# Optimization experiments

Hardware: AMD Instinct MI355X
Metric: run time of the kernel (lower is better)

Reference implementation:

```python
import jax, jax.numpy as jnp
import numpy as np
import math

D_MODEL = 1024
NUM_HEADS = 16
D_K = D_MODEL // NUM_HEADS
MAX_SEQ_LEN = 2048
THETA = 10000.0


def _make_rope_tables():
    inv_freq = 1.0 / (THETA ** (np.arange(0, D_K, 2, dtype=np.float32) / D_K))  # [D_K/2]
    pos = np.arange(MAX_SEQ_LEN, dtype=np.float32)
    freqs = np.einsum('i,j->ij', pos, inv_freq)                 # [S, D_K/2]
    dfreq = np.repeat(freqs, 2, axis=-1)                        # [S, D_K] (interleaved)
    return jnp.asarray(np.cos(dfreq)), jnp.asarray(np.sin(dfreq))


def setup_inputs() -> dict:
    key = jax.random.key(0)
    ks = jax.random.split(key, 5)
    std = math.sqrt(2.0 / (D_MODEL + D_MODEL))
    x = jax.random.normal(ks[0], (2, 2048, D_MODEL), dtype=jnp.float32)
    Wq = jax.random.truncated_normal(ks[1], -3.0, 3.0, (D_MODEL, D_MODEL), jnp.float32) * std
    Wk = jax.random.truncated_normal(ks[2], -3.0, 3.0, (D_MODEL, D_MODEL), jnp.float32) * std
    Wv = jax.random.truncated_normal(ks[3], -3.0, 3.0, (D_MODEL, D_MODEL), jnp.float32) * std
    Wo = jax.random.truncated_normal(ks[4], -3.0, 3.0, (D_MODEL, D_MODEL), jnp.float32) * std
    cos, sin = _make_rope_tables()
    token_positions = jnp.arange(2048, dtype=jnp.int32)
    return {"x": x, "Wq": Wq, "Wk": Wk, "Wv": Wv, "Wo": Wo,
            "cos": cos, "sin": sin, "token_positions": token_positions}


def _apply_rope(t, cos, sin, pos):
    # t: [B, H, S, D_K]; cos/sin gathered to [S, D_K], broadcast over B,H
    c = cos[pos]
    s = sin[pos]
    t1 = t[..., 0::2]
    t2 = t[..., 1::2]
    rot = jnp.stack((-t2, t1), axis=-1).reshape(t.shape)
    return t * c + rot * s


def reference(x, Wq, Wk, Wv, Wo, cos, sin, token_positions):
    B, S, _ = x.shape
    def heads(W):
        return (x @ W.T).reshape(B, S, NUM_HEADS, D_K).transpose(0, 2, 1, 3)  # [B,H,S,Dk]
    q = _apply_rope(heads(Wq), cos, sin, token_positions)
    k = _apply_rope(heads(Wk), cos, sin, token_positions)
    v = heads(Wv)
    scores = jnp.einsum('bhqd,bhkd->bhqk', q, k) / math.sqrt(D_K)
    causal = jnp.tril(jnp.ones((S, S), dtype=bool))
    scores = jnp.where(causal, scores, -jnp.inf)
    attn = jax.nn.softmax(scores, axis=-1)
    out = jnp.einsum('bhqk,bhkd->bhqd', attn, v)
    out = out.transpose(0, 2, 1, 3).reshape(B, S, D_MODEL)
    return out @ Wo.T
```

## Files before the change

### kernel.cpp

```cpp
#include <hip/hip_runtime.h>
#include <cstdint>
#include <cstddef>

#define D_MODEL 1024
#define NH 16
#define DK 64
#define S_LEN 2048

typedef __attribute__((ext_vector_type(8))) short bf16x8;
typedef __attribute__((ext_vector_type(4))) float f32x4;

#define QSCALE 0.1803368801111204f

__device__ __forceinline__ unsigned short f2bf(float f) {
    union { float f; unsigned int u; } v; v.f = f;
    unsigned int r = (v.u + 0x7fffu + ((v.u >> 16) & 1u)) >> 16;
    return (unsigned short)r;
}

#define GLL(g, l) __builtin_amdgcn_global_load_lds( \
    (const __attribute__((address_space(1))) unsigned int*)(g), \
    (__attribute__((address_space(3))) unsigned int*)(l), 16, 0, 0)

__global__ __launch_bounds__(256) void convert_bf16(
    const float* __restrict__ x,
    const float* __restrict__ wq, const float* __restrict__ wk,
    const float* __restrict__ wv, const float* __restrict__ wo,
    unsigned short* __restrict__ Xb, unsigned short* __restrict__ Wb,
    unsigned short* __restrict__ Wob)
{
    const unsigned t = blockIdx.x * 256 + threadIdx.x;
    const float* src;
    unsigned short* dst;
    if (t < 1048576u)      { src = x  + 4 * (size_t)t;               dst = Xb  + 4 * (size_t)t; }
    else if (t < 1310720u) { size_t i = t - 1048576u; src = wq + 4*i; dst = Wb + 4*i; }
    else if (t < 1572864u) { size_t i = t - 1310720u; src = wk + 4*i; dst = Wb + 1048576u + 4*i; }
    else if (t < 1835008u) { size_t i = t - 1572864u; src = wv + 4*i; dst = Wb + 2097152u + 4*i; }
    else                   { size_t i = t - 1835008u; src = wo + 4*i; dst = Wob + 4*i; }
    float4 v = *(const float4*)src;
    unsigned short pk[4] = {f2bf(v.x), f2bf(v.y), f2bf(v.z), f2bf(v.w)};
    *(uint2*)dst = *(const uint2*)pk;
}


#define CP 132
__global__ __launch_bounds__(256) void gemm_qkv(
    const unsigned short* __restrict__ Xb, const unsigned short* __restrict__ Wb,
    const float* __restrict__ cosT, const float* __restrict__ sinT,
    const int* __restrict__ posArr,
    unsigned short* __restrict__ Qo, unsigned short* __restrict__ Ko,
    unsigned short* __restrict__ Vt)
{
    __shared__ __align__(16) unsigned short smem[4 * 128 * 64];
    unsigned short* Cs = smem;

    const int tid  = threadIdx.x;
    const int wave = tid >> 6;
    const int lane = tid & 63;
    const int m16  = lane & 15;
    const int quad = lane >> 4;
    const int warpM = (wave >> 1) * 64;
    const int warpN = (wave & 1) * 64;
    const int rowBase = blockIdx.y * 128;
    const int colBase = blockIdx.x * 128;

    const int l8  = lane >> 3;
    const int lb  = lane & 7;
    const int cbl = (lb ^ l8) * 8;

    const unsigned short* Arow = Xb + (size_t)rowBase * D_MODEL;
    const unsigned short* Brow = Wb + (size_t)colBase * D_MODEL;

    f32x4 acc[4][4];
#pragma unroll
    for (int i = 0; i < 4; ++i)
#pragma unroll
        for (int j = 0; j < 4; ++j) acc[i][j] = (f32x4){0.f, 0.f, 0.f, 0.f};

    auto stage = [&](int k0, int bsel) {
        unsigned short* As = smem + bsel * 16384;
        unsigned short* Bs = As + 8192;
#pragma unroll
        for (int it = 0; it < 4; ++it) {
            const int r = wave * 32 + it * 8 + l8;
            const int dstOff = wave * 2048 + it * 512 + lane * 8;
            GLL(Arow + (size_t)r * D_MODEL + k0 + cbl, &As[dstOff]);
            GLL(Brow + (size_t)r * D_MODEL + k0 + cbl, &Bs[dstOff]);
        }
    };

    stage(0, 0);
    for (int it = 0; it < 16; ++it) {
        const int cur = it & 1;
        if (it < 15) {
            stage((it + 1) * 64, cur ^ 1);
            __asm__ volatile("s_waitcnt vmcnt(8)" ::: "memory");
        } else {
            __asm__ volatile("s_waitcnt vmcnt(0)" ::: "memory");
        }
        __syncthreads();
        const unsigned short* As = smem + cur * 16384;
        const unsigned short* Bs = As + 8192;
#pragma unroll
        for (int ks = 0; ks < 2; ++ks) {
            bf16x8 af[4], bf[4];
#pragma unroll
            for (int t4 = 0; t4 < 4; ++t4) {
                const int rowA = warpM + t4 * 16 + m16;
                const int rowB = warpN + t4 * 16 + m16;
                const int cb = ((ks * 4 + quad) ^ (m16 & 7)) * 8;
                af[t4] = *(const bf16x8*)&As[rowA * 64 + cb];
                bf[t4] = *(const bf16x8*)&Bs[rowB * 64 + cb];
            }
#pragma unroll
            for (int mt = 0; mt < 4; ++mt)
#pragma unroll
                for (int nt = 0; nt < 4; ++nt)
                    acc[mt][nt] = __builtin_amdgcn_mfma_f32_16x16x32_bf16(
                        af[mt], bf[nt], acc[mt][nt], 0, 0, 0);
        }
        __syncthreads();
    }

    const int which = (colBase + warpN) >> 10;
    if (which == 2) {
#pragma unroll
        for (int mt = 0; mt < 4; ++mt) {
            const int gr0 = rowBase + warpM + mt * 16 + quad * 4;
            const int b   = gr0 >> 11;
            const int s0  = gr0 & 2047;
#pragma unroll
            for (int nt = 0; nt < 4; ++nt) {
                const int c1 = (colBase + warpN + nt * 16 + m16) & 1023;
                const int h  = c1 >> 6;
                const int d  = c1 & 63;
                unsigned short pk[4];
#pragma unroll
                for (int r = 0; r < 4; ++r) pk[r] = f2bf(acc[mt][nt][r]);
                *(uint2*)(Vt + ((size_t)(b * NH + h) * DK + d) * S_LEN + s0) =
                    *(const uint2*)pk;
            }
        }
    } else {
#pragma unroll
        for (int mt = 0; mt < 4; ++mt) {
            const int lr0 = warpM + mt * 16 + quad * 4;
#pragma unroll
            for (int nt = 0; nt < 4; ++nt) {
                const int lc = warpN + nt * 16 + m16;
                const int d  = lc & 63;
#pragma unroll
                for (int r = 0; r < 4; ++r) {
                    const int s = (rowBase + lr0 + r) & 2047;
                    const int p = posArr[s];
                    float v = acc[mt][nt][r];
                    float o = __shfl_xor(v, 1, 64);
                    float c  = cosT[(size_t)p * DK + d];
                    float sn = sinT[(size_t)p * DK + d];
                    float res = (d & 1) ? (v * c + o * sn) : (v * c - o * sn);
                    if (which == 0) res *= QSCALE;
                    Cs[(lr0 + r) * CP + lc] = f2bf(res);
                }
            }
        }
        __syncthreads();
        unsigned short* outB = (which == 0) ? Qo : Ko;
        const int r2   = tid >> 1;
        const int half = tid & 1;
        const int gr   = rowBase + r2;
        const int b    = gr >> 11;
        const int s    = gr & 2047;
        const int h    = ((colBase & 1023) + half * 64) >> 6;
        unsigned short* dst = outB + ((size_t)(b * NH + h) * S_LEN + s) * DK;
        const unsigned short* srcp = &Cs[r2 * CP + half * 64];
#pragma unroll
        for (int j = 0; j < 8; ++j)
            ((uint4*)dst)[j] = ((const uint4*)srcp)[j];
    }
}

__global__ __launch_bounds__(256) void gemm_proj(
    const unsigned short* __restrict__ A, const unsigned short* __restrict__ B,
    float* __restrict__ C)
{
    __shared__ __align__(16) unsigned short smem[4 * 128 * 64];

    const int tid  = threadIdx.x;
    const int wave = tid >> 6;
    const int lane = tid & 63;
    const int m16  = lane & 15;
    const int quad = lane >> 4;
    const int warpM = (wave >> 1) * 64;
    const int warpN = (wave & 1) * 64;
    const int rowBase = blockIdx.y * 128;
    const int colBase = blockIdx.x * 128;

    const int l8  = lane >> 3;
    const int lb  = lane & 7;
    const int cbl = (lb ^ l8) * 8;

    const unsigned short* Arow = A + (size_t)rowBase * D_MODEL;
    const unsigned short* Brow = B + (size_t)colBase * D_MODEL;

    f32x4 acc[4][4];
#pragma unroll
    for (int i = 0; i < 4; ++i)
#pragma unroll
        for (int j = 0; j < 4; ++j) acc[i][j] = (f32x4){0.f, 0.f, 0.f, 0.f};

    auto stage = [&](int k0, int bsel) {
        unsigned short* As = smem + bsel * 16384;
        unsigned short* Bs = As + 8192;
#pragma unroll
        for (int it = 0; it < 4; ++it) {
            const int r = wave * 32 + it * 8 + l8;
            const int dstOff = wave * 2048 + it * 512 + lane * 8;
            GLL(Arow + (size_t)r * D_MODEL + k0 + cbl, &As[dstOff]);
            GLL(Brow + (size_t)r * D_MODEL + k0 + cbl, &Bs[dstOff]);
        }
    };

    stage(0, 0);
    for (int it = 0; it < 16; ++it) {
        const int cur = it & 1;
        if (it < 15) {
            stage((it + 1) * 64, cur ^ 1);
            __asm__ volatile("s_waitcnt vmcnt(8)" ::: "memory");
        } else {
            __asm__ volatile("s_waitcnt vmcnt(0)" ::: "memory");
        }
        __syncthreads();
        const unsigned short* As = smem + cur * 16384;
        const unsigned short* Bs = As + 8192;
#pragma unroll
        for (int ks = 0; ks < 2; ++ks) {
            bf16x8 af[4], bf[4];
#pragma unroll
            for (int t4 = 0; t4 < 4; ++t4) {
                const int rowA = warpM + t4 * 16 + m16;
                const int rowB = warpN + t4 * 16 + m16;
                const int cb = ((ks * 4 + quad) ^ (m16 & 7)) * 8;
                af[t4] = *(const bf16x8*)&As[rowA * 64 + cb];
                bf[t4] = *(const bf16x8*)&Bs[rowB * 64 + cb];
            }
#pragma unroll
            for (int mt = 0; mt < 4; ++mt)
#pragma unroll
                for (int nt = 0; nt < 4; ++nt)
                    acc[mt][nt] = __builtin_amdgcn_mfma_f32_16x16x32_bf16(
                        af[mt], bf[nt], acc[mt][nt], 0, 0, 0);
        }
        __syncthreads();
    }

#pragma unroll
    for (int mt = 0; mt < 4; ++mt)
#pragma unroll
        for (int reg = 0; reg < 4; ++reg) {
            int gr = rowBase + warpM + mt * 16 + quad * 4 + reg;
            float* crow = C + (size_t)gr * D_MODEL + colBase + warpN;
#pragma unroll
            for (int nt = 0; nt < 4; ++nt)
                crow[nt * 16 + m16] = acc[mt][nt][reg];
        }
}

__global__ __launch_bounds__(256, 3) void flash_mfma(
    const unsigned short* __restrict__ Q,
    const unsigned short* __restrict__ K,
    const unsigned short* __restrict__ Vt,
    unsigned short* __restrict__ O)
{
    const int g    = blockIdx.x;
    const int qt   = 31 - (g >> 5);
    const int bh   = g & 31;
    const int b    = bh >> 4;
    const int h    = bh & 15;
    const int tid  = threadIdx.x;
    const int wave = tid >> 6;
    const int lane = tid & 63;
    const int m16  = lane & 15;
    const int quad = lane >> 4;
    const int l8   = lane >> 3;
    const int nIter = (qt >> 1) + 1;

    __shared__ __align__(16) unsigned short Ks[128 * 64];
    __shared__ __align__(16) unsigned short VsT[64 * 128];
    __shared__ __align__(16) unsigned short Ps[64][136];

    const unsigned short* Qg = Q + ((size_t)bh * S_LEN + qt * 64) * DK;
#pragma unroll
    for (int it = 0; it < 2; ++it) {
        const int rb = wave * 16 + it * 8;
        const int r  = rb + l8;
        const int cb = ((lane & 7) ^ (r & 7)) * 8;
        GLL(Qg + r * DK + cb, &Ks[rb * 64 + lane * 8]);
    }
    __asm__ volatile("s_waitcnt vmcnt(0)" ::: "memory");
    __syncthreads();
    const int qrow = wave * 16 + m16;
    const bf16x8 qf0 = *(const bf16x8*)&Ks[qrow * 64 + ((quad ^ (m16 & 7)) * 8)];
    const bf16x8 qf1 = *(const bf16x8*)&Ks[qrow * 64 + (((4 + quad) ^ (m16 & 7)) * 8)];

    const short one_bf = (short)0x3F80;
    const bf16x8 ones8 = {one_bf, one_bf, one_bf, one_bf,
                          one_bf, one_bf, one_bf, one_bf};

    f32x4 o[4];
    f32x4 lacc = (f32x4){0.f, 0.f, 0.f, 0.f};
#pragma unroll
    for (int r = 0; r < 4; ++r) o[r] = (f32x4){0.f, 0.f, 0.f, 0.f};

    const unsigned short* Kg0 = K + (size_t)bh * S_LEN * DK;
    const unsigned short* Vg0 = Vt + (size_t)bh * DK * S_LEN;

    for (int kb = 0; kb < nIter; ++kb) {
        const int ko = kb * 128;
        __syncthreads();
#pragma unroll
        for (int it = 0; it < 4; ++it) {
            const int rb = wave * 32 + it * 8;
            const int r  = rb + l8;
            const int cb = ((lane & 7) ^ (r & 7)) * 8;
            GLL(Kg0 + (size_t)(ko + r) * DK + cb, &Ks[rb * 64 + lane * 8]);
        }
#pragma unroll
        for (int it = 0; it < 4; ++it) {
            const int db = wave * 16 + it * 4;
            const int d  = db + (lane >> 4);
            const int cb = ((lane & 15) ^ (d & 15)) * 8;
            GLL(Vg0 + (size_t)d * S_LEN + ko + cb, &VsT[db * 128 + lane * 8]);
        }
        __asm__ volatile("s_waitcnt vmcnt(0)" ::: "memory");
        __syncthreads();

        f32x4 s[8];
#pragma unroll
        for (int ct = 0; ct < 8; ++ct) {
            const int kr = ct * 16 + m16;
            bf16x8 kf0 = *(const bf16x8*)&Ks[kr * 64 + ((quad ^ (m16 & 7)) * 8)];
            bf16x8 kf1 = *(const bf16x8*)&Ks[kr * 64 + (((4 + quad) ^ (m16 & 7)) * 8)];
            f32x4 z = {0.f, 0.f, 0.f, 0.f};
            z = __builtin_amdgcn_mfma_f32_16x16x32_bf16(qf0, kf0, z, 0, 0, 0);
            z = __builtin_amdgcn_mfma_f32_16x16x32_bf16(qf1, kf1, z, 0, 0, 0);
            s[ct] = z;
        }

        if (kb == nIter - 1) {
#pragma unroll
            for (int ct = 0; ct < 8; ++ct)
#pragma unroll
                for (int r = 0; r < 4; ++r) {
                    int colk = ko + ct * 16 + m16;
                    int row  = qt * 64 + wave * 16 + quad * 4 + r;
                    if (colk > row) s[ct][r] = -16384.f;
                }
        }

#pragma unroll
        for (int ct = 0; ct < 8; ++ct)
#pragma unroll
            for (int r = 0; r < 4; ++r)
                Ps[wave * 16 + quad * 4 + r][ct * 16 + m16] =
                    f2bf(__builtin_exp2f(s[ct][r]));

        __asm__ volatile("s_waitcnt lgkmcnt(0)" ::: "memory");

        bf16x8 pf[4];
#pragma unroll
        for (int kc = 0; kc < 4; ++kc)
            pf[kc] = *(const bf16x8*)&Ps[wave * 16 + m16][kc * 32 + quad * 8];
#pragma unroll
        for (int kc = 0; kc < 4; ++kc)
            lacc = __builtin_amdgcn_mfma_f32_16x16x32_bf16(pf[kc], ones8, lacc, 0, 0, 0);
#pragma unroll
        for (int ct = 0; ct < 4; ++ct) {
            const int vr = ct * 16 + m16;
#pragma unroll
            for (int kc = 0; kc < 4; ++kc) {
                bf16x8 vf = *(const bf16x8*)
                    &VsT[vr * 128 + (((kc * 4 + quad) ^ m16) * 8)];
                o[ct] = __builtin_amdgcn_mfma_f32_16x16x32_bf16(pf[kc], vf, o[ct], 0, 0, 0);
            }
        }
    }

    float inv[4];
#pragma unroll
    for (int r = 0; r < 4; ++r) inv[r] = 1.0f / lacc[r];
#pragma unroll
    for (int r = 0; r < 4; ++r) {
        int srow = qt * 64 + wave * 16 + quad * 4 + r;
        unsigned short* orow = O + (((size_t)b * S_LEN + srow) * NH + h) * DK;
#pragma unroll
        for (int ct = 0; ct < 4; ++ct)
            orow[ct * 16 + m16] = f2bf(o[ct][r] * inv[r]);
    }
}

extern "C" void kernel_launch(void* const* d_in, const int* in_sizes, int n_in,
                              void* d_out, int out_size, void* d_ws, size_t ws_size,
                              hipStream_t stream)
{
    const float* x      = (const float*)d_in[0];
    const float* Wq     = (const float*)d_in[1];
    const float* Wk     = (const float*)d_in[2];
    const float* Wv     = (const float*)d_in[3];
    const float* Wo     = (const float*)d_in[4];
    const float* cosT   = (const float*)d_in[5];
    const float* sinT   = (const float*)d_in[6];
    const int*   posArr = (const int*)d_in[7];
    float* out = (float*)d_out;

    unsigned short* ws0 = (unsigned short*)d_ws;
    unsigned short* Xb  = ws0;
    unsigned short* Wb  = ws0 + 4194304;
    unsigned short* Wob = ws0 + 7340032;
    unsigned short* Qw  = ws0 + 8388608;
    unsigned short* Kw  = ws0 + 12582912;
    unsigned short* Vtw = ws0 + 16777216;
    unsigned short* Ow  = ws0 + 20971520;

    convert_bf16<<<8192, 256, 0, stream>>>(x, Wq, Wk, Wv, Wo, Xb, Wb, Wob);

    gemm_qkv<<<dim3(3072 / 128, 4096 / 128), 256, 0, stream>>>(
        Xb, Wb, cosT, sinT, posArr, Qw, Kw, Vtw);

    flash_mfma<<<1024, 256, 0, stream>>>(Qw, Kw, Vtw, Ow);

    gemm_proj<<<dim3(D_MODEL / 128, 4096 / 128), 256, 0, stream>>>(Ow, Wob, out);
}
```

Baseline: 201.5 us.

## Split long causal query tiles across two KV chunks and merge partials

The flash attention kernel now splits the eight longest query tiles per head into two KV-range chunks, launching 1280 blocks instead of 1024, with split tiles scheduled between the longest unsplit ones. Split blocks write unnormalized fp32 partial outputs and row sums to workspace, and a new merge kernel sums them and normalizes. This relies on the softmax using no running max, so partials add directly. It aims to shorten the tail from the heaviest causal blocks at the cost of an extra launch and fp32 partial traffic.

```diff
diff --git a/kernel.cpp b/kernel.cpp
--- a/kernel.cpp
+++ b/kernel.cpp
@@ -269,20 +269,38 @@
     const unsigned short* __restrict__ Q,
     const unsigned short* __restrict__ K,
     const unsigned short* __restrict__ Vt,
-    unsigned short* __restrict__ O)
+    unsigned short* __restrict__ O,
+    float* __restrict__ oP, float* __restrict__ lP)
 {
-    const int g    = blockIdx.x;
-    const int qt   = 31 - (g >> 5);
-    const int bh   = g & 31;
-    const int b    = bh >> 4;
-    const int h    = bh & 15;
+    const int g  = blockIdx.x;
+    const int j  = g >> 5;
+    const int bh = g & 31;
+    const int b  = bh >> 4;
+    const int h  = bh & 15;
+
+    int qt, kb0, kb1, chunk;
+    bool split;
+    if (j < 8) {
+        split = false; chunk = 0; qt = 23 - j;
+        kb0 = 0; kb1 = (qt >> 1) + 1;
+    } else if (j < 24) {
+        split = true; const int jj = j - 8;
+        qt = 24 + (jj >> 1); chunk = jj & 1;
+        const int nIt = (qt >> 1) + 1;
+        const int c0  = nIt >> 1;
+        kb0 = chunk ? c0 : 0; kb1 = chunk ? nIt : c0;
+    } else {
+        split = false; chunk = 0; qt = 39 - j;
+        kb0 = 0; kb1 = (qt >> 1) + 1;
+    }
+    const int nIterFull = (qt >> 1) + 1;
+
     const int tid  = threadIdx.x;
     const int wave = tid >> 6;
     const int lane = tid & 63;
     const int m16  = lane & 15;
     const int quad = lane >> 4;
     const int l8   = lane >> 3;
-    const int nIter = (qt >> 1) + 1;
 
     __shared__ __align__(16) unsigned short Ks[128 * 64];
     __shared__ __align__(16) unsigned short VsT[64 * 128];
@@ -314,7 +332,7 @@
     const unsigned short* Kg0 = K + (size_t)bh * S_LEN * DK;
     const unsigned short* Vg0 = Vt + (size_t)bh * DK * S_LEN;
 
-    for (int kb = 0; kb < nIter; ++kb) {
+    for (int kb = kb0; kb < kb1; ++kb) {
         const int ko = kb * 128;
         __syncthreads();
 #pragma unroll
@@ -346,7 +364,7 @@
             s[ct] = z;
         }
 
-        if (kb == nIter - 1) {
+        if (kb == nIterFull - 1) {
 #pragma unroll
             for (int ct = 0; ct < 8; ++ct)
 #pragma unroll
@@ -385,17 +403,64 @@
         }
     }
 
-    float inv[4];
-#pragma unroll
-    for (int r = 0; r < 4; ++r) inv[r] = 1.0f / lacc[r];
-#pragma unroll
-    for (int r = 0; r < 4; ++r) {
-        int srow = qt * 64 + wave * 16 + quad * 4 + r;
-        unsigned short* orow = O + (((size_t)b * S_LEN + srow) * NH + h) * DK;
-#pragma unroll
-        for (int ct = 0; ct < 4; ++ct)
-            orow[ct * 16 + m16] = f2bf(o[ct][r] * inv[r]);
-    }
+    if (!split) {
+        float inv[4];
+#pragma unroll
+        for (int r = 0; r < 4; ++r) inv[r] = 1.0f / lacc[r];
+#pragma unroll
+        for (int r = 0; r < 4; ++r) {
+            int srow = qt * 64 + wave * 16 + quad * 4 + r;
+            unsigned short* orow = O + (((size_t)b * S_LEN + srow) * NH + h) * DK;
+#pragma unroll
+            for (int ct = 0; ct < 4; ++ct)
+                orow[ct * 16 + m16] = f2bf(o[ct][r] * inv[r]);
+        }
+    } else {
+        const int slot = bh * 8 + (qt - 24);
+        float* ob = oP + ((size_t)chunk * 256 + slot) * 4096;
+        float* lb = lP + ((size_t)chunk * 256 + slot) * 64;
+#pragma unroll
+        for (int r = 0; r < 4; ++r) {
+            const int row = wave * 16 + quad * 4 + r;
+#pragma unroll
+            for (int ct = 0; ct < 4; ++ct)
+                ob[row * 64 + ct * 16 + m16] = o[ct][r];
+            if (m16 == 0) lb[row] = lacc[r];
+        }
+    }
+}
+
+__global__ __launch_bounds__(256) void flash_merge(
+    const float* __restrict__ oP, const float* __restrict__ lP,
+    unsigned short* __restrict__ O)
+{
+    const int slot = blockIdx.x;
+    const int bh   = slot >> 3;
+    const int qt   = (slot & 7) + 24;
+    const int b    = bh >> 4;
+    const int h    = bh & 15;
+    const int t    = threadIdx.x;
+    const int row  = t >> 2;
+    const int dp   = (t & 3) * 16;
+
+    const float* oA = oP + (size_t)slot * 4096 + row * 64 + dp;
+    const float* oB = oP + (size_t)(256 + slot) * 4096 + row * 64 + dp;
+    const float inv = 1.0f / (lP[slot * 64 + row] + lP[(256 + slot) * 64 + row]);
+
+    unsigned short pk[16];
+#pragma unroll
+    for (int i = 0; i < 16; i += 4) {
+        float4 a  = *(const float4*)(oA + i);
+        float4 bb = *(const float4*)(oB + i);
+        pk[i + 0] = f2bf((a.x + bb.x) * inv);
+        pk[i + 1] = f2bf((a.y + bb.y) * inv);
+        pk[i + 2] = f2bf((a.z + bb.z) * inv);
+        pk[i + 3] = f2bf((a.w + bb.w) * inv);
+    }
+    const int srow = qt * 64 + row;
+    unsigned short* dst = O + (((size_t)b * S_LEN + srow) * NH + h) * DK + dp;
+    ((uint4*)dst)[0] = ((const uint4*)pk)[0];
+    ((uint4*)dst)[1] = ((const uint4*)pk)[1];
 }
 
 extern "C" void kernel_launch(void* const* d_in, const int* in_sizes, int n_in,
@@ -420,13 +485,16 @@
     unsigned short* Kw  = ws0 + 12582912;
     unsigned short* Vtw = ws0 + 16777216;
     unsigned short* Ow  = ws0 + 20971520;
+    float* oP = (float*)(ws0 + 25165824);
+    float* lP = oP + 2 * 256 * 4096;
 
     convert_bf16<<<8192, 256, 0, stream>>>(x, Wq, Wk, Wv, Wo, Xb, Wb, Wob);
 
     gemm_qkv<<<dim3(3072 / 128, 4096 / 128), 256, 0, stream>>>(
         Xb, Wb, cosT, sinT, posArr, Qw, Kw, Vtw);
 
-    flash_mfma<<<1024, 256, 0, stream>>>(Qw, Kw, Vtw, Ow);
+    flash_mfma<<<1280, 256, 0, stream>>>(Qw, Kw, Vtw, Ow, oP, lP);
+    flash_merge<<<256, 256, 0, stream>>>(oP, lP, Ow);
 
     gemm_proj<<<dim3(D_MODEL / 128, 4096 / 128), 256, 0, stream>>>(Ow, Wob, out);
 }
```

Measured after the change: 204.3 us. No clear change (+1.4%).

## Keep softmax probabilities in registers by transposing the QK^T MFMA

Applied to the files above, without the earlier changes.

Swaps the MFMA operands for S = QK^T so each lane holds a column-major fragment of P that can feed the PV MFMA directly as the A operand. The P shared-memory buffer and its store/reload round trip are dropped, and PV plus the row-sum are moved to the 16x16x16 bf16 MFMA with 4-element operands. The lower LDS use lets launch bounds go from 3 to 4 blocks per CU. In exchange there are twice as many, smaller MFMAs and V fragment loads, and more register pressure under the tighter occupancy bound.

```diff
diff --git a/kernel.cpp b/kernel.cpp
--- a/kernel.cpp
+++ b/kernel.cpp
@@ -8,6 +8,7 @@
 #define S_LEN 2048
 
 typedef __attribute__((ext_vector_type(8))) short bf16x8;
+typedef __attribute__((ext_vector_type(4))) short bf16x4;
 typedef __attribute__((ext_vector_type(4))) float f32x4;
 
 #define QSCALE 0.1803368801111204f
@@ -265,7 +266,7 @@
         }
 }
 
-__global__ __launch_bounds__(256, 3) void flash_mfma(
+__global__ __launch_bounds__(256, 4) void flash_mfma(
     const unsigned short* __restrict__ Q,
     const unsigned short* __restrict__ K,
     const unsigned short* __restrict__ Vt,
@@ -286,7 +287,6 @@
 
     __shared__ __align__(16) unsigned short Ks[128 * 64];
     __shared__ __align__(16) unsigned short VsT[64 * 128];
-    __shared__ __align__(16) unsigned short Ps[64][136];
 
     const unsigned short* Qg = Q + ((size_t)bh * S_LEN + qt * 64) * DK;
 #pragma unroll
@@ -303,8 +303,7 @@
     const bf16x8 qf1 = *(const bf16x8*)&Ks[qrow * 64 + (((4 + quad) ^ (m16 & 7)) * 8)];
 
     const short one_bf = (short)0x3F80;
-    const bf16x8 ones8 = {one_bf, one_bf, one_bf, one_bf,
-                          one_bf, one_bf, one_bf, one_bf};
+    const bf16x4 ones4 = {one_bf, one_bf, one_bf, one_bf};
 
     f32x4 o[4];
     f32x4 lacc = (f32x4){0.f, 0.f, 0.f, 0.f};
@@ -341,46 +340,47 @@
             bf16x8 kf0 = *(const bf16x8*)&Ks[kr * 64 + ((quad ^ (m16 & 7)) * 8)];
             bf16x8 kf1 = *(const bf16x8*)&Ks[kr * 64 + (((4 + quad) ^ (m16 & 7)) * 8)];
             f32x4 z = {0.f, 0.f, 0.f, 0.f};
-            z = __builtin_amdgcn_mfma_f32_16x16x32_bf16(qf0, kf0, z, 0, 0, 0);
-            z = __builtin_amdgcn_mfma_f32_16x16x32_bf16(qf1, kf1, z, 0, 0, 0);
+            z = __builtin_amdgcn_mfma_f32_16x16x32_bf16(kf0, qf0, z, 0, 0, 0);
+            z = __builtin_amdgcn_mfma_f32_16x16x32_bf16(kf1, qf1, z, 0, 0, 0);
             s[ct] = z;
         }
 
         if (kb == nIter - 1) {
+            const int qg = qt * 64 + wave * 16 + m16;
 #pragma unroll
             for (int ct = 0; ct < 8; ++ct)
 #pragma unroll
                 for (int r = 0; r < 4; ++r) {
-                    int colk = ko + ct * 16 + m16;
-                    int row  = qt * 64 + wave * 16 + quad * 4 + r;
-                    if (colk > row) s[ct][r] = -16384.f;
+                    const int key = ko + ct * 16 + quad * 4 + r;
+                    if (key > qg) s[ct][r] = -16384.f;
                 }
         }
 
+        bf16x4 pf[8];
+#pragma unroll
+        for (int ct = 0; ct < 8; ++ct) {
+            bf16x4 pk;
+#pragma unroll
+            for (int r = 0; r < 4; ++r)
+                pk[r] = (short)f2bf(__builtin_exp2f(s[ct][r]));
+            pf[ct] = pk;
+        }
+
 #pragma unroll
         for (int ct = 0; ct < 8; ++ct)
-#pragma unroll
-            for (int r = 0; r < 4; ++r)
-                Ps[wave * 16 + quad * 4 + r][ct * 16 + m16] =
-                    f2bf(__builtin_exp2f(s[ct][r]));
-
-        __asm__ volatile("s_waitcnt lgkmcnt(0)" ::: "memory");
-
-        bf16x8 pf[4];
-#pragma unroll
-        for (int kc = 0; kc < 4; ++kc)
-            pf[kc] = *(const bf16x8*)&Ps[wave * 16 + m16][kc * 32 + quad * 8];
-#pragma unroll
-        for (int kc = 0; kc < 4; ++kc)
-            lacc = __builtin_amdgcn_mfma_f32_16x16x32_bf16(pf[kc], ones8, lacc, 0, 0, 0);
-#pragma unroll
-        for (int ct = 0; ct < 4; ++ct) {
-            const int vr = ct * 16 + m16;
-#pragma unroll
-            for (int kc = 0; kc < 4; ++kc) {
-                bf16x8 vf = *(const bf16x8*)
-                    &VsT[vr * 128 + (((kc * 4 + quad) ^ m16) * 8)];
-                o[ct] = __builtin_amdgcn_mfma_f32_16x16x32_bf16(pf[kc], vf, o[ct], 0, 0, 0);
+            lacc = __builtin_amdgcn_mfma_f32_16x16x16bf16_1k(
+                pf[ct], ones4, lacc, 0, 0, 0);
+
+#pragma unroll
+        for (int dt = 0; dt < 4; ++dt) {
+            const int vrow = dt * 16 + m16;
+#pragma unroll
+            for (int ct = 0; ct < 8; ++ct) {
+                const int chunk = ct * 2 + (quad >> 1);
+                const int off = ((chunk ^ m16) * 8) + (quad & 1) * 4;
+                bf16x4 vf = *(const bf16x4*)&VsT[vrow * 128 + off];
+                o[dt] = __builtin_amdgcn_mfma_f32_16x16x16bf16_1k(
+                    pf[ct], vf, o[dt], 0, 0, 0);
             }
         }
     }
@@ -390,11 +390,11 @@
     for (int r = 0; r < 4; ++r) inv[r] = 1.0f / lacc[r];
 #pragma unroll
     for (int r = 0; r < 4; ++r) {
-        int srow = qt * 64 + wave * 16 + quad * 4 + r;
+        const int srow = qt * 64 + wave * 16 + quad * 4 + r;
         unsigned short* orow = O + (((size_t)b * S_LEN + srow) * NH + h) * DK;
 #pragma unroll
-        for (int ct = 0; ct < 4; ++ct)
-            orow[ct * 16 + m16] = f2bf(o[ct][r] * inv[r]);
+        for (int dt = 0; dt < 4; ++dt)
+            orow[dt * 16 + m16] = f2bf(o[dt][r] * inv[r]);
     }
 }
 
```

Measured after the change: 206.5 us. 2.5% more time.
